# Performance work log

Hardware: AMD Instinct MI355X
Metric: run time of the kernel (lower is better)

Reference implementation:

```python
import jax, jax.numpy as jnp
import numpy as np

N, M, D = 8192, 8192, 256
GAMMA = 1.0 / D  # standard RBF bandwidth gamma = 1/D


def setup_inputs() -> dict:
    key = jax.random.key(0)
    kx, ks = jax.random.split(key)
    x = jax.random.normal(kx, (N, D), dtype=jnp.float32)
    support = jax.random.normal(ks, (M, D), dtype=jnp.float32)
    return {"x": x, "support": support}


def reference(x, support):
    # Vectorized RBF Gram matrix: K[i, j] = exp(-gamma * ||x_i - s_j||^2)
    # ||x_i - s_j||^2 = ||x_i||^2 + ||s_j||^2 - 2 x_i . s_j  (cdist-style, one GEMM)
    x_sq = jnp.sum(x * x, axis=-1, keepdims=True)            # [N, 1]
    s_sq = jnp.sum(support * support, axis=-1)[None, :]      # [1, M]
    cross = jnp.einsum('nd,md->nm', x, support)              # [N, M]
    sq_dists = jnp.maximum(x_sq + s_sq - 2.0 * cross, 0.0)   # clamp fp error
    return jnp.exp(-GAMMA * sq_dists)
```

## Files before the change

### kernel.cpp

```cpp
#include <hip/hip_runtime.h>

#define N 8192
#define M 8192
#define D 256

typedef unsigned short ushort_t;
typedef __attribute__((ext_vector_type(8))) short short8;
typedef __attribute__((ext_vector_type(4))) float floatx4;

__device__ __forceinline__ unsigned short f2bf(float f) {
  unsigned int u = __float_as_uint(f);
  u += 0x7fffu + ((u >> 16) & 1u);
  return (unsigned short)(u >> 16);
}

__global__ __launch_bounds__(256) void prep_kernel(const float* __restrict__ x,
                                                   const float* __restrict__ s,
                                                   ushort_t* __restrict__ xb,
                                                   ushort_t* __restrict__ sb,
                                                   float* __restrict__ xn,
                                                   float* __restrict__ sn) {
  int gw = blockIdx.x * 4 + (threadIdx.x >> 6);
  int lane = threadIdx.x & 63;
  const float* src;
  ushort_t* dst;
  float* nrm;
  int row;
  if (gw < N) { src = x; dst = xb; nrm = xn; row = gw; }
  else        { src = s; dst = sb; nrm = sn; row = gw - N; }
  float4 v = ((const float4*)(src + (size_t)row * D))[lane];
  float ss = v.x * v.x + v.y * v.y + v.z * v.z + v.w * v.w;
  ushort4 o;
  o.x = f2bf(v.x); o.y = f2bf(v.y); o.z = f2bf(v.z); o.w = f2bf(v.w);
  *(ushort4*)(dst + (size_t)row * D + lane * 4) = o;
#pragma unroll
  for (int off = 32; off > 0; off >>= 1) ss += __shfl_down(ss, off);
  if (lane == 0) nrm[row] = ss;
}

__global__ __launch_bounds__(256, 2) void rbf_gemm(const ushort_t* __restrict__ X,
                                                   const ushort_t* __restrict__ S,
                                                   const float* __restrict__ xn,
                                                   const float* __restrict__ sn,
                                                   float* __restrict__ out) {
  __shared__ __attribute__((aligned(16))) ushort_t As[4 * 128 * 32];
  __shared__ __attribute__((aligned(16))) ushort_t Bs[4 * 128 * 32];
  __shared__ float xnS[128];
  __shared__ float snS[128];

  const int tid = threadIdx.x;
  const int lane = tid & 63;
  const int wave = tid >> 6;
  const int bx = blockIdx.x;
  const int by = blockIdx.y;

  if (tid < 128) xnS[tid] = xn[by * 128 + tid];
  else           snS[tid - 128] = sn[bx * 128 + (tid - 128)];

  const int wr = (wave >> 1) * 64;
  const int wc = (wave & 1) * 64;

  const int srow = wave * 32 + (lane >> 2);
  const int scol = (lane & 3) * 8;
  const ushort_t* gA = X + (size_t)(by * 128 + srow) * D + scol;
  const ushort_t* gB = S + (size_t)(bx * 128 + srow) * D + scol;

  const int q4 = lane >> 4;
  const int m16 = lane & 15;

  floatx4 acc[4][4];
#pragma unroll
  for (int i = 0; i < 4; ++i)
#pragma unroll
    for (int j = 0; j < 4; ++j) acc[i][j] = (floatx4){0.f, 0.f, 0.f, 0.f};

#pragma unroll
  for (int r = 0; r < 2; ++r) {
    const int kb = r * 128;
    __syncthreads();
#pragma unroll
    for (int c = 0; c < 4; ++c) {
      const int k0 = kb + c * 32;
      ushort_t* lA = As + c * 4096 + wave * 1024;
      ushort_t* lB = Bs + c * 4096 + wave * 1024;
      __builtin_amdgcn_global_load_lds(
          (const __attribute__((address_space(1))) void*)(gA + k0),
          (__attribute__((address_space(3))) void*)(lA), 16, 0, 0);
      __builtin_amdgcn_global_load_lds(
          (const __attribute__((address_space(1))) void*)(gA + (size_t)16 * D + k0),
          (__attribute__((address_space(3))) void*)(lA + 512), 16, 0, 0);
      __builtin_amdgcn_global_load_lds(
          (const __attribute__((address_space(1))) void*)(gB + k0),
          (__attribute__((address_space(3))) void*)(lB), 16, 0, 0);
      __builtin_amdgcn_global_load_lds(
          (const __attribute__((address_space(1))) void*)(gB + (size_t)16 * D + k0),
          (__attribute__((address_space(3))) void*)(lB + 512), 16, 0, 0);
    }
    __syncthreads();

#pragma unroll
    for (int c = 0; c < 4; ++c) {
      const ushort_t* cA = As + c * 4096;
      const ushort_t* cB = Bs + c * 4096;
      short8 a_frag[4], b_frag[4];
#pragma unroll
      for (int i = 0; i < 4; ++i)
        a_frag[i] = *(const short8*)(cA + (wr + i * 16 + m16) * 32 + q4 * 8);
#pragma unroll
      for (int j = 0; j < 4; ++j)
        b_frag[j] = *(const short8*)(cB + (wc + j * 16 + m16) * 32 + q4 * 8);
#pragma unroll
      for (int i = 0; i < 4; ++i)
#pragma unroll
        for (int j = 0; j < 4; ++j)
          acc[i][j] = __builtin_amdgcn_mfma_f32_16x16x32_bf16(a_frag[i], b_frag[j],
                                                              acc[i][j], 0, 0, 0);
    }
  }

  const float cexp = -1.0f / (float)D;
#pragma unroll
  for (int i = 0; i < 4; ++i) {
#pragma unroll
    for (int j = 0; j < 4; ++j) {
#pragma unroll
      for (int r = 0; r < 4; ++r) {
        const int rl = wr + i * 16 + q4 * 4 + r;
        const int cl = wc + j * 16 + m16;
        float sq = xnS[rl] + snS[cl] - 2.0f * acc[i][j][r];
        sq = fmaxf(sq, 0.0f);
        out[(size_t)(by * 128 + rl) * M + (bx * 128 + cl)] = __expf(cexp * sq);
      }
    }
  }
}

extern "C" void kernel_launch(void* const* d_in, const int* in_sizes, int n_in,
                              void* d_out, int out_size, void* d_ws, size_t ws_size,
                              hipStream_t stream) {
  const float* x = (const float*)d_in[0];
  const float* s = (const float*)d_in[1];
  float* out = (float*)d_out;
  char* ws = (char*)d_ws;
  ushort_t* xb = (ushort_t*)ws;
  ushort_t* sb = (ushort_t*)(ws + (size_t)N * D * 2);
  float* xn = (float*)(ws + (size_t)(N + M) * D * 2);
  float* sn = xn + N;

  prep_kernel<<<(N + M) / 4, 256, 0, stream>>>(x, s, xb, sb, xn, sn);
  dim3 grid(M / 128, N / 128);
  rbf_gemm<<<grid, 256, 0, stream>>>(xb, sb, xn, sn, out);
}
```

Before: 294.9 us.

## Factor RBF exponent into per-row exps and halve LDS staging for occupancy

The row and column norm terms are moved into the prep kernel as exp(-||v||^2/D), so the epilogue computes exS*esS*exp(2/D*dot) and clamps the result to 1. The K-loop now stages 64 columns per iteration instead of 128, which halves shared memory, and launch bounds ask for 4 blocks per CU instead of 2. The goal is more resident waves to hide global-store and load latency, plus a lighter epilogue. The cost is twice as many barrier/load rounds, possible register spilling under the tighter bound, and a numerical change: the product of separate exponentials can underflow or overflow differently from the original clamped distance form.

```diff
diff --git a/kernel.cpp b/kernel.cpp
--- a/kernel.cpp
+++ b/kernel.cpp
@@ -18,16 +18,16 @@
                                                    const float* __restrict__ s,
                                                    ushort_t* __restrict__ xb,
                                                    ushort_t* __restrict__ sb,
-                                                   float* __restrict__ xn,
-                                                   float* __restrict__ sn) {
+                                                   float* __restrict__ xe,
+                                                   float* __restrict__ se) {
   int gw = blockIdx.x * 4 + (threadIdx.x >> 6);
   int lane = threadIdx.x & 63;
   const float* src;
   ushort_t* dst;
   float* nrm;
   int row;
-  if (gw < N) { src = x; dst = xb; nrm = xn; row = gw; }
-  else        { src = s; dst = sb; nrm = sn; row = gw - N; }
+  if (gw < N) { src = x; dst = xb; nrm = xe; row = gw; }
+  else        { src = s; dst = sb; nrm = se; row = gw - N; }
   float4 v = ((const float4*)(src + (size_t)row * D))[lane];
   float ss = v.x * v.x + v.y * v.y + v.z * v.z + v.w * v.w;
   ushort4 o;
@@ -35,18 +35,18 @@
   *(ushort4*)(dst + (size_t)row * D + lane * 4) = o;
 #pragma unroll
   for (int off = 32; off > 0; off >>= 1) ss += __shfl_down(ss, off);
-  if (lane == 0) nrm[row] = ss;
+  if (lane == 0) nrm[row] = __expf(ss * (-1.0f / (float)D));
 }
 
-__global__ __launch_bounds__(256, 2) void rbf_gemm(const ushort_t* __restrict__ X,
+__global__ __launch_bounds__(256, 4) void rbf_gemm(const ushort_t* __restrict__ X,
                                                    const ushort_t* __restrict__ S,
-                                                   const float* __restrict__ xn,
-                                                   const float* __restrict__ sn,
+                                                   const float* __restrict__ xe,
+                                                   const float* __restrict__ se,
                                                    float* __restrict__ out) {
-  __shared__ __attribute__((aligned(16))) ushort_t As[4 * 128 * 32];
-  __shared__ __attribute__((aligned(16))) ushort_t Bs[4 * 128 * 32];
-  __shared__ float xnS[128];
-  __shared__ float snS[128];
+  __shared__ __attribute__((aligned(16))) ushort_t As[2 * 128 * 32];
+  __shared__ __attribute__((aligned(16))) ushort_t Bs[2 * 128 * 32];
+  __shared__ float exS[128];
+  __shared__ float esS[128];
 
   const int tid = threadIdx.x;
   const int lane = tid & 63;
@@ -54,8 +54,8 @@
   const int bx = blockIdx.x;
   const int by = blockIdx.y;
 
-  if (tid < 128) xnS[tid] = xn[by * 128 + tid];
-  else           snS[tid - 128] = sn[bx * 128 + (tid - 128)];
+  if (tid < 128) exS[tid] = xe[by * 128 + tid];
+  else           esS[tid - 128] = se[bx * 128 + (tid - 128)];
 
   const int wr = (wave >> 1) * 64;
   const int wc = (wave & 1) * 64;
@@ -75,11 +75,11 @@
     for (int j = 0; j < 4; ++j) acc[i][j] = (floatx4){0.f, 0.f, 0.f, 0.f};
 
 #pragma unroll
-  for (int r = 0; r < 2; ++r) {
-    const int kb = r * 128;
+  for (int r = 0; r < 4; ++r) {
+    const int kb = r * 64;
     __syncthreads();
 #pragma unroll
-    for (int c = 0; c < 4; ++c) {
+    for (int c = 0; c < 2; ++c) {
       const int k0 = kb + c * 32;
       ushort_t* lA = As + c * 4096 + wave * 1024;
       ushort_t* lB = Bs + c * 4096 + wave * 1024;
@@ -99,7 +99,7 @@
     __syncthreads();
 
 #pragma unroll
-    for (int c = 0; c < 4; ++c) {
+    for (int c = 0; c < 2; ++c) {
       const ushort_t* cA = As + c * 4096;
       const ushort_t* cB = Bs + c * 4096;
       short8 a_frag[4], b_frag[4];
@@ -118,18 +118,18 @@
     }
   }
 
-  const float cexp = -1.0f / (float)D;
+  const float c2 = 2.0f / (float)D;
 #pragma unroll
   for (int i = 0; i < 4; ++i) {
 #pragma unroll
     for (int j = 0; j < 4; ++j) {
+      const int cl = wc + j * 16 + m16;
+      const float es_v = esS[cl];
 #pragma unroll
       for (int r = 0; r < 4; ++r) {
         const int rl = wr + i * 16 + q4 * 4 + r;
-        const int cl = wc + j * 16 + m16;
-        float sq = xnS[rl] + snS[cl] - 2.0f * acc[i][j][r];
-        sq = fmaxf(sq, 0.0f);
-        out[(size_t)(by * 128 + rl) * M + (bx * 128 + cl)] = __expf(cexp * sq);
+        float k = exS[rl] * es_v * __expf(c2 * acc[i][j][r]);
+        out[(size_t)(by * 128 + rl) * M + (bx * 128 + cl)] = fminf(k, 1.0f);
       }
     }
   }
@@ -144,10 +144,10 @@
   char* ws = (char*)d_ws;
   ushort_t* xb = (ushort_t*)ws;
   ushort_t* sb = (ushort_t*)(ws + (size_t)N * D * 2);
-  float* xn = (float*)(ws + (size_t)(N + M) * D * 2);
-  float* sn = xn + N;
+  float* xe = (float*)(ws + (size_t)(N + M) * D * 2);
+  float* se = xe + N;
 
-  prep_kernel<<<(N + M) / 4, 256, 0, stream>>>(x, s, xb, sb, xn, sn);
+  prep_kernel<<<(N + M) / 4, 256, 0, stream>>>(x, s, xb, sb, xe, se);
   dim3 grid(M / 128, N / 128);
-  rbf_gemm<<<grid, 256, 0, stream>>>(xb, sb, xn, sn, out);
+  rbf_gemm<<<grid, 256, 0, stream>>>(xb, sb, xe, se, out);
 }
```

Result: slower. 354.6 us (+20.3%).
